# Optimization experiments

Measured on AMD Instinct MI355X. Metric: run time of the kernel, lower is better.

Reference implementation:

```python
import jax, jax.numpy as jnp
import numpy as np

N, E, HID, ED, L, H, D = 65536, 262144, 256, 64, 2, 8, 32
FF = 4 * HID
A_START = 8192  # first action gripper node; nodes [A_START:] are the T*K action nodes


def _ln(x, s, b, eps=1e-5):
    mu = jnp.mean(x, -1, keepdims=True)
    var = jnp.var(x, -1, keepdims=True)
    return (x - mu) * jax.lax.rsqrt(var + eps) * s + b


def _gnn_forward(x, edge_attr, edge_index, Wq, Wk, Wv, WeK, WeV, Wo,
                 ln1_s, ln1_b, ffn_w1, ffn_b1, ffn_w2, ffn_b2, ln2_s, ln2_b):
    # Hetero graph transformer over the single ('gripper','action','gripper') relation:
    # per-layer edge-indexed gather -> multi-head attention with edge features ->
    # segment softmax over incoming edges -> scatter-aggregate -> residual/LN/FFN.
    n = x.shape[0]
    e = edge_attr.shape[0]
    src, dst = edge_index[0], edge_index[1]
    inv_sqrt_d = np.float32(1.0 / np.sqrt(D))
    for l in range(Wq.shape[0]):
        q = (x @ Wq[l]).reshape(n, H, D)
        k = (x @ Wk[l]).reshape(n, H, D)
        v = (x @ Wv[l]).reshape(n, H, D)
        kj = k[src] + (edge_attr @ WeK[l]).reshape(e, H, D)  # [E,H,D] gathered keys + edge bias
        vj = v[src] + (edge_attr @ WeV[l]).reshape(e, H, D)
        score = jnp.einsum('ehd,ehd->eh', q[dst], kj) * inv_sqrt_d  # [E,H]
        smax = jax.ops.segment_max(score, dst, num_segments=n)
        p = jnp.exp(score - smax[dst])
        denom = jax.ops.segment_sum(p, dst, num_segments=n)
        alpha = p / denom[dst]  # segment softmax over incoming edges
        agg = jax.ops.segment_sum((alpha[..., None] * vj).reshape(e, H * D), dst, num_segments=n)
        x = _ln(x + agg @ Wo[l], ln1_s[l], ln1_b[l])
        hid = jax.nn.gelu(x @ ffn_w1[l] + ffn_b1[l], approximate=False) @ ffn_w2[l] + ffn_b2[l]
        x = _ln(x + hid, ln2_s[l], ln2_b[l])
    return x


def setup_inputs() -> dict:
    key = jax.random.key(0)
    ks = iter(jax.random.split(key, 16))
    w = lambda shape: jax.random.normal(next(ks), shape, jnp.float32) * 0.05
    return {
        "all_gripper_feats": jax.random.normal(next(ks), (N, HID), jnp.float32),
        "edge_attr": jax.random.normal(next(ks), (E, ED), jnp.float32),
        "Wq": w((L, HID, H * D)), "Wk": w((L, HID, H * D)), "Wv": w((L, HID, H * D)),
        "WeK": w((L, ED, H * D)), "WeV": w((L, ED, H * D)), "Wo": w((L, H * D, HID)),
        "ln1_s": jnp.ones((L, HID), jnp.float32), "ln1_b": jnp.zeros((L, HID), jnp.float32),
        "ffn_w1": w((L, HID, FF)), "ffn_b1": jnp.zeros((L, FF), jnp.float32),
        "ffn_w2": w((L, FF, HID)), "ffn_b2": jnp.zeros((L, HID), jnp.float32),
        "ln2_s": jnp.ones((L, HID), jnp.float32), "ln2_b": jnp.zeros((L, HID), jnp.float32),
        "head_w1": w((HID, HID)), "head_b1": jnp.zeros((HID,), jnp.float32),
        "head_w2": w((HID, 7)), "head_b2": jnp.zeros((7,), jnp.float32),
        "edge_index": jax.random.randint(next(ks), (2, E), 0, N),
        "action_start": A_START,
    }


def reference(all_gripper_feats, edge_attr, Wq, Wk, Wv, WeK, WeV, Wo,
              ln1_s, ln1_b, ffn_w1, ffn_b1, ffn_w2, ffn_b2, ln2_s, ln2_b,
              head_w1, head_b1, head_w2, head_b2, edge_index, action_start):
    x = _gnn_forward(all_gripper_feats, edge_attr, edge_index, Wq, Wk, Wv, WeK, WeV, Wo,
                     ln1_s, ln1_b, ffn_w1, ffn_b1, ffn_w2, ffn_b2, ln2_s, ln2_b)
    a = x[action_start:]  # action gripper nodes (T*K, hidden)
    return jax.nn.gelu(a @ head_w1 + head_b1, approximate=False) @ head_w2 + head_b2  # (T*K, 7)
```

## Files before the change

kernel.cpp:

```cpp
#include <hip/hip_runtime.h>
#include <hip/hip_bf16.h>
#include <math.h>

#define NN     65536
#define NE     262144
#define HIDN   256
#define EDIM   64
#define NHEAD  8
#define FFN    1024
#define ASTART 8192
#define NACT   (NN - ASTART)
#define NCH    32768
#define NCHUNK (NE / NCH)
#define DPC    (NN / NCHUNK)
#define RCH    32768

typedef __attribute__((ext_vector_type(8))) short short8;
typedef __attribute__((ext_vector_type(4))) short short4v;
typedef __attribute__((ext_vector_type(4))) float float4v;
typedef __hip_bfloat16 bf16;

__device__ __forceinline__ float b2f(short s) {
    union { unsigned u; float f; } c;
    c.u = ((unsigned)(unsigned short)s) << 16;
    return c.f;
}
__device__ __forceinline__ short f2b(float f) {
    __hip_bfloat16 h = __float2bfloat16(f);
    return *reinterpret_cast<short*>(&h);
}
__device__ __forceinline__ float gelu_fast(float v) {
    const float x  = v * 0.70710678118654752f;
    const float ax = fabsf(x);
    const float t  = __builtin_amdgcn_rcpf(1.0f + 0.3275911f * ax);
    const float y  = t * (0.254829592f + t * (-0.284496736f + t * (1.421413741f +
                     t * (-1.453152027f + t * 1.061405429f))));
    const float e  = __expf(-x * x);
    float erf = 1.0f - y * e;
    erf = copysignf(erf, x);
    return 0.5f * v * (1.0f + erf);
}
__device__ __forceinline__ void gload16(const void* g, void* l) {
    __builtin_amdgcn_global_load_lds(
        (const __attribute__((address_space(1))) void*)(uintptr_t)g,
        (__attribute__((address_space(3))) void*)(unsigned)(uintptr_t)l,
        16, 0, 0);
}

__global__ void convert_kernel(const float* __restrict__ src,
                               bf16* __restrict__ dst, int n) {
    int i = blockIdx.x * 256 + threadIdx.x;
    if (i < n) dst[i] = __float2bfloat16(src[i]);
}
__global__ void convert4_kernel(const float* __restrict__ src,
                                bf16* __restrict__ dst, int n4) {
    int i = blockIdx.x * 256 + threadIdx.x;
    if (i >= n4) return;
    float4v f = *(const float4v*)(src + (size_t)i * 4);
    short4v o;
    #pragma unroll
    for (int j = 0; j < 4; ++j) o[j] = f2b(f[j]);
    *(short4v*)((short*)dst + (size_t)i * 4) = o;
}

__global__ void transpose_kernel(const float* __restrict__ src,
                                 bf16* __restrict__ dst, int R, int Cc) {
    int idx = blockIdx.x * 256 + threadIdx.x;
    if (idx >= R * Cc) return;
    int r = idx / Cc, c = idx - r * Cc;
    dst[(size_t)c * R + r] = __float2bfloat16(src[idx]);
}

__global__ void hist_kernel(const int* __restrict__ dstI, int* __restrict__ cnt) {
    int i = blockIdx.x * 256 + threadIdx.x;
    if (i < NE) atomicAdd(&cnt[dstI[i]], 1);
}
__global__ void scan1_kernel(const int* __restrict__ cnt, int* __restrict__ rp,
                             int* __restrict__ bsum) {
    __shared__ int s[256];
    int t = threadIdx.x, i = blockIdx.x * 256 + t;
    int v = cnt[i]; s[t] = v; __syncthreads();
    for (int off = 1; off < 256; off <<= 1) {
        int x = (t >= off) ? s[t - off] : 0; __syncthreads();
        s[t] += x; __syncthreads();
    }
    rp[i] = s[t] - v;
    if (t == 255) bsum[blockIdx.x] = s[255];
}
__global__ void scan2_kernel(int* __restrict__ bsum) {
    __shared__ int s[256];
    int t = threadIdx.x; int v = bsum[t]; s[t] = v; __syncthreads();
    for (int off = 1; off < 256; off <<= 1) {
        int x = (t >= off) ? s[t - off] : 0; __syncthreads();
        s[t] += x; __syncthreads();
    }
    bsum[t] = s[t] - v;
}
__global__ void scan3_kernel(int* __restrict__ rp, const int* __restrict__ bsum,
                             int* __restrict__ cursor) {
    int i = blockIdx.x * 256 + threadIdx.x;
    int v = rp[i] + bsum[i >> 8];
    rp[i] = v; cursor[i] = v;
    if (i == 0) rp[NN] = NE;
}
__global__ void scatter_kernel(const int* __restrict__ srcI, const int* __restrict__ dstI,
                               int* __restrict__ cursor, int* __restrict__ perm,
                               int* __restrict__ src_s, int* __restrict__ dst_s) {
    int e = blockIdx.x * 256 + threadIdx.x;
    if (e >= NE) return;
    int d = dstI[e];
    int pos = atomicAdd(&cursor[d], 1);
    perm[pos] = e; src_s[pos] = srcI[e]; dst_s[pos] = d;
}

template<int AMODE, bool DO_GELU>
__global__ __launch_bounds__(256) void gemm_kernel(
    const void* __restrict__ A,
    const bf16* __restrict__ BT,
    const bf16* __restrict__ bias,
    bf16* __restrict__ C,
    int M, int Nn, int K,
    const int* __restrict__ perm)
{
    __shared__ __align__(16) short As[2][128 * 32];
    __shared__ __align__(16) short Bs[2][128 * 32];

    const int gx   = gridDim.x;
    const int nwg  = gx * gridDim.y;
    const int orig = blockIdx.y * gx + blockIdx.x;
    const int q8   = nwg >> 3, r8 = nwg & 7;
    const int xcd  = orig & 7, rk = orig >> 3;
    const int nid  = (xcd < r8 ? xcd * (q8 + 1) : r8 * (q8 + 1) + (xcd - r8) * q8) + rk;
    const int by   = nid / gx;
    const int bx   = nid - by * gx;

    const int t    = threadIdx.x;
    const int wave = t >> 6;
    const int lane = t & 63;
    const int l15  = lane & 15;
    const int quad = lane >> 4;
    const int wm   = (wave & 1) * 64;
    const int wn   = (wave >> 1) * 64;
    const int bm   = by * 128;
    const int bn   = bx * 128;
    const int srow = t >> 2;
    const int sw   = srow & 3;
    const int scolB = ((t & 3) ^ sw) * 8;
    const int scolA = (t & 3) * 8;

    const short* Ab = (const short*)A  + (size_t)(bm + srow) * K + scolB;
    const short* Bb = (const short*)BT + (size_t)(bn + srow) * K + scolB;
    const float* Af0 = nullptr;
    const float* Af1 = nullptr;
    if (AMODE == 1) {
        Af0 = (const float*)A + (size_t)(bm + srow) * K + scolA;
        Af1 = Af0 + (size_t)64 * K;
    } else if (AMODE == 2) {
        const int pr0 = perm[bm + srow];
        const int pr1 = perm[bm + 64 + srow];
        Af0 = (const float*)A + (size_t)pr0 * K + scolA;
        Af1 = (const float*)A + (size_t)pr1 * K + scolA;
    }
    const int offW  = wave * 1024;
    const int offTs = (t * 16) ^ (sw << 4);
    const int qs16  = (quad ^ (l15 & 3)) * 16;

    float4v acc[4][4];
    #pragma unroll
    for (int i = 0; i < 4; ++i)
        #pragma unroll
        for (int j = 0; j < 4; ++j) acc[i][j] = (float4v){0.f, 0.f, 0.f, 0.f};

    const int nt = K >> 5;

    auto STAGE = [&](int b, int k0) {
        char* lA = (char*)As[b];
        char* lB = (char*)Bs[b];
        if (AMODE == 0) {
            gload16(Ab + k0,                  lA + offW);
            gload16(Ab + (size_t)64 * K + k0, lA + 4096 + offW);
        } else {
            #pragma unroll
            for (int i = 0; i < 2; ++i) {
                const float* s = (i ? Af1 : Af0) + k0;
                float4v f0 = *(const float4v*)s;
                float4v f1 = *(const float4v*)(s + 4);
                short8 w;
                #pragma unroll
                for (int j = 0; j < 4; ++j) { w[j] = f2b(f0[j]); w[4 + j] = f2b(f1[j]); }
                *(short8*)(lA + i * 4096 + offTs) = w;
            }
        }
        gload16(Bb + k0,                  lB + offW);
        gload16(Bb + (size_t)64 * K + k0, lB + 4096 + offW);
    };

    STAGE(0, 0);
    __syncthreads();

    for (int kt = 0; kt < nt; ++kt) {
        const int cur = kt & 1;
        if (kt + 1 < nt) STAGE(cur ^ 1, (kt + 1) * 32);

        const char* lA = (const char*)As[cur];
        const char* lB = (const char*)Bs[cur];
        short8 afr[4], bfr[4];
        #pragma unroll
        for (int i = 0; i < 4; ++i)
            afr[i] = *(const short8*)(lA + (wm + i * 16 + l15) * 64 + qs16);
        #pragma unroll
        for (int j = 0; j < 4; ++j)
            bfr[j] = *(const short8*)(lB + (wn + j * 16 + l15) * 64 + qs16);
        #pragma unroll
        for (int i = 0; i < 4; ++i)
            #pragma unroll
            for (int j = 0; j < 4; ++j)
                acc[i][j] = __builtin_amdgcn_mfma_f32_16x16x32_bf16(afr[i], bfr[j], acc[i][j], 0, 0, 0);
        __syncthreads();
    }

    #pragma unroll
    for (int j = 0; j < 4; ++j) {
        const int col = bn + wn + j * 16 + l15;
        const float bv = bias ? b2f(((const short*)bias)[col]) : 0.0f;
        #pragma unroll
        for (int i = 0; i < 4; ++i) {
            const int row0 = bm + wm + i * 16 + quad * 4;
            #pragma unroll
            for (int r = 0; r < 4; ++r) {
                float v = acc[i][j][r] + bv;
                if (DO_GELU) v = gelu_fast(v);
                C[(size_t)(row0 + r) * Nn + col] = __float2bfloat16(v);
            }
        }
    }
}

__global__ __launch_bounds__(256) void score_kernel(
    const bf16* __restrict__ q, const bf16* __restrict__ k,
    const bf16* __restrict__ eK,
    const int* __restrict__ src_s, const int* __restrict__ dst_s,
    short* __restrict__ pbuf, int e0, int qkstride)
{
    const int p = e0 + blockIdx.x * 4 + (threadIdx.x >> 6);
    const int lane = threadIdx.x & 63;
    const int s = src_s[p], d = dst_s[p];
    const int off = lane * 4;

    const short4v qv = *(const short4v*)((const short*)q  + (size_t)d * qkstride + off);
    const short4v kv = *(const short4v*)((const short*)k  + (size_t)s * qkstride + off);
    const short4v ev = *(const short4v*)((const short*)eK + (size_t)(p - e0) * HIDN + off);
    float x = 0.f;
    #pragma unroll
    for (int j = 0; j < 4; ++j) x += b2f(qv[j]) * (b2f(kv[j]) + b2f(ev[j]));
    x += __shfl_xor(x, 1);
    x += __shfl_xor(x, 2);
    x += __shfl_xor(x, 4);
    if ((lane & 7) == 0) {
        const float sc = fminf(fmaxf(x * 0.17677669529663689f, -30.f), 30.f);
        pbuf[(size_t)p * NHEAD + (lane >> 3)] = f2b(expf(sc));
    }
}

__global__ __launch_bounds__(256) void agg_kernel(
    const short* __restrict__ pbuf, const bf16* __restrict__ v,
    const bf16* __restrict__ eV,
    const int* __restrict__ src_s, const int* __restrict__ rp,
    float* __restrict__ agg, int e0, int e1, int dlo)
{
    const int d = dlo + blockIdx.x * 4 + (threadIdx.x >> 6);
    const int lane = threadIdx.x & 63;
    const int es = rp[d], ee = rp[d + 1];
    const int lo = es > e0 ? es : e0;
    const int hi = ee < e1 ? ee : e1;
    if (lo >= hi) return;
    const int h = lane >> 3, off = lane * 4;

    float den = 0.f;
    for (int p = es; p < ee; ++p) den += b2f(pbuf[(size_t)p * NHEAD + h]);

    float a0 = 0.f, a1 = 0.f, a2 = 0.f, a3 = 0.f;
    for (int p = lo; p < hi; ++p) {
        const float al = b2f(pbuf[(size_t)p * NHEAD + h]) / den;
        const int s = src_s[p];
        const short4v vv = *(const short4v*)((const short*)v  + (size_t)s * HIDN + off);
        const short4v ev = *(const short4v*)((const short*)eV + (size_t)(p - e0) * HIDN + off);
        a0 += al * (b2f(vv[0]) + b2f(ev[0]));
        a1 += al * (b2f(vv[1]) + b2f(ev[1]));
        a2 += al * (b2f(vv[2]) + b2f(ev[2]));
        a3 += al * (b2f(vv[3]) + b2f(ev[3]));
    }
    float* ao = agg + (size_t)d * HIDN + off;
    if (es >= e0 && ee <= e1) {
        *(float4v*)ao = (float4v){a0, a1, a2, a3};
    } else {
        atomicAdd(ao + 0, a0); atomicAdd(ao + 1, a1);
        atomicAdd(ao + 2, a2); atomicAdd(ao + 3, a3);
    }
}

__global__ __launch_bounds__(256) void ln_kernel(
    bf16* __restrict__ x, const bf16* __restrict__ t,
    const bf16* __restrict__ sc, const bf16* __restrict__ bi, int r0)
{
    const int row = r0 + blockIdx.x * 4 + (threadIdx.x >> 6);
    const int lane = threadIdx.x & 63;
    const size_t base = (size_t)row * HIDN + lane * 4;
    const size_t tbase = (size_t)(row - r0) * HIDN + lane * 4;
    const short4v xv = *(const short4v*)((const short*)x + base);
    const short4v tv = *(const short4v*)((const short*)t + tbase);
    float v[4];
    #pragma unroll
    for (int j = 0; j < 4; ++j) v[j] = b2f(xv[j]) + b2f(tv[j]);
    float sum = v[0] + v[1] + v[2] + v[3];
    float ssq = v[0]*v[0] + v[1]*v[1] + v[2]*v[2] + v[3]*v[3];
    #pragma unroll
    for (int m = 1; m < 64; m <<= 1) { sum += __shfl_xor(sum, m); ssq += __shfl_xor(ssq, m); }
    const float mean = sum * (1.0f / 256.0f);
    const float var  = fmaxf(ssq * (1.0f / 256.0f) - mean * mean, 0.0f);
    const float rstd = rsqrtf(var + 1e-5f);
    const short4v sv = *(const short4v*)((const short*)sc + lane * 4);
    const short4v bv = *(const short4v*)((const short*)bi + lane * 4);
    short4v out;
    #pragma unroll
    for (int j = 0; j < 4; ++j)
        out[j] = f2b((v[j] - mean) * rstd * b2f(sv[j]) + b2f(bv[j]));
    *(short4v*)((short*)x + base) = out;
}

__global__ __launch_bounds__(256) void head2_kernel(
    const bf16* __restrict__ h1, const bf16* __restrict__ w2T,
    const bf16* __restrict__ b2, float* __restrict__ out)
{
    const int row = blockIdx.x * 4 + (threadIdx.x >> 6);
    const int lane = threadIdx.x & 63;
    const int off = lane * 4;
    const short4v hv = *(const short4v*)((const short*)h1 + (size_t)row * HIDN + off);
    float hf[4];
    #pragma unroll
    for (int j = 0; j < 4; ++j) hf[j] = b2f(hv[j]);
    float acc[7];
    #pragma unroll
    for (int jc = 0; jc < 7; ++jc) {
        const short4v wv = *(const short4v*)((const short*)w2T + jc * HIDN + off);
        float a = hf[0]*b2f(wv[0]) + hf[1]*b2f(wv[1]) + hf[2]*b2f(wv[2]) + hf[3]*b2f(wv[3]);
        #pragma unroll
        for (int m = 1; m < 64; m <<= 1) a += __shfl_xor(a, m);
        acc[jc] = a;
    }
    if (lane < 7) {
        float r = lane == 0 ? acc[0] : lane == 1 ? acc[1] : lane == 2 ? acc[2] :
                  lane == 3 ? acc[3] : lane == 4 ? acc[4] : lane == 5 ? acc[5] : acc[6];
        out[(size_t)row * 7 + lane] = r + b2f(((const short*)b2)[lane]);
    }
}

extern "C" void kernel_launch(void* const* d_in, const int* in_sizes, int n_in,
                              void* d_out, int out_size, void* d_ws, size_t ws_size,
                              hipStream_t stream)
{
    const float* xin   = (const float*)d_in[0];
    const float* eattr = (const float*)d_in[1];
    const float* Wq    = (const float*)d_in[2];
    const float* Wk    = (const float*)d_in[3];
    const float* Wv    = (const float*)d_in[4];
    const float* WeK   = (const float*)d_in[5];
    const float* WeV   = (const float*)d_in[6];
    const float* Wo    = (const float*)d_in[7];
    const float* ln1s  = (const float*)d_in[8];
    const float* ln1b  = (const float*)d_in[9];
    const float* fw1   = (const float*)d_in[10];
    const float* fb1   = (const float*)d_in[11];
    const float* fw2   = (const float*)d_in[12];
    const float* fb2   = (const float*)d_in[13];
    const float* ln2s  = (const float*)d_in[14];
    const float* ln2b  = (const float*)d_in[15];
    const float* hw1   = (const float*)d_in[16];
    const float* hb1   = (const float*)d_in[17];
    const float* hw2   = (const float*)d_in[18];
    const float* hb2   = (const float*)d_in[19];
    const int*  eidx   = (const int*)d_in[20];
    const int*  srcI   = eidx;
    const int*  dstI   = eidx + NE;

    char* base = (char*)d_ws;
    size_t off = 0;
    auto carve = [&](size_t bytes) -> char* {
        char* p = base + off;
        off += (bytes + 255) & ~(size_t)255;
        return p;
    };
    bf16*  x_b    = (bf16*) carve((size_t)NN * HIDN * 2);
    bf16*  qk_b   = (bf16*) carve((size_t)NN * 2 * HIDN * 2);
    bf16*  v_b    = (bf16*) carve((size_t)NN * HIDN * 2);
    bf16*  echunk = (bf16*) carve((size_t)NCH * HIDN * 2);
    short* pbuf   = (short*)carve((size_t)NE * NHEAD * 2);
    int*   perm   = (int*)  carve((size_t)NE * 4);
    int*   src_s  = (int*)  carve((size_t)NE * 4);
    int*   dst_s  = (int*)  carve((size_t)NE * 4);
    int*   rowp   = (int*)  carve((size_t)(NN + 1) * 4);
    bf16*  WqkT   = (bf16*) carve((size_t)2 * HIDN * HIDN * 2);
    bf16*  WvT    = (bf16*) carve((size_t)HIDN * HIDN * 2);
    bf16*  WoT    = (bf16*) carve((size_t)HIDN * HIDN * 2);
    bf16*  WeKT   = (bf16*) carve((size_t)HIDN * EDIM * 2);
    bf16*  WeVT   = (bf16*) carve((size_t)HIDN * EDIM * 2);
    bf16*  W1T    = (bf16*) carve((size_t)FFN * HIDN * 2);
    bf16*  W2T    = (bf16*) carve((size_t)HIDN * FFN * 2);
    bf16*  HW1T   = (bf16*) carve((size_t)HIDN * HIDN * 2);
    bf16*  HW2T   = (bf16*) carve((size_t)8 * HIDN * 2);
    bf16*  c_ln1s = (bf16*) carve((size_t)2 * HIDN * 2);
    bf16*  c_ln1b = (bf16*) carve((size_t)2 * HIDN * 2);
    bf16*  c_ln2s = (bf16*) carve((size_t)2 * HIDN * 2);
    bf16*  c_ln2b = (bf16*) carve((size_t)2 * HIDN * 2);
    bf16*  c_fb1  = (bf16*) carve((size_t)2 * FFN * 2);
    bf16*  c_fb2  = (bf16*) carve((size_t)2 * HIDN * 2);
    bf16*  c_hb1  = (bf16*) carve((size_t)HIDN * 2);
    bf16*  c_hb2  = (bf16*) carve((size_t)16 * 2);
    if (off > ws_size) return;

    int* cnt    = (int*)echunk;
    int* cursor = cnt + NN;
    int* bsum   = cursor + NN;
    float* agg    = (float*)qk_b;
    bf16*  tmp_b  = v_b;
    bf16*  hid    = qk_b;
    bf16*  ffnout = v_b;

    const int TB = 256;
    #define GRID1(n) dim3(((n) + TB - 1) / TB)

    convert4_kernel<<<GRID1(NN * HIDN / 4), TB, 0, stream>>>(xin, x_b, NN * HIDN / 4);
    convert_kernel<<<GRID1(2 * HIDN), TB, 0, stream>>>(ln1s, c_ln1s, 2 * HIDN);
    convert_kernel<<<GRID1(2 * HIDN), TB, 0, stream>>>(ln1b, c_ln1b, 2 * HIDN);
    convert_kernel<<<GRID1(2 * HIDN), TB, 0, stream>>>(ln2s, c_ln2s, 2 * HIDN);
    convert_kernel<<<GRID1(2 * HIDN), TB, 0, stream>>>(ln2b, c_ln2b, 2 * HIDN);
    convert_kernel<<<GRID1(2 * FFN), TB, 0, stream>>>(fb1, c_fb1, 2 * FFN);
    convert_kernel<<<GRID1(2 * HIDN), TB, 0, stream>>>(fb2, c_fb2, 2 * HIDN);
    convert_kernel<<<GRID1(HIDN), TB, 0, stream>>>(hb1, c_hb1, HIDN);
    convert_kernel<<<1, TB, 0, stream>>>(hb2, c_hb2, 7);
    transpose_kernel<<<GRID1(HIDN * HIDN), TB, 0, stream>>>(hw1, HW1T, HIDN, HIDN);
    transpose_kernel<<<GRID1(HIDN * 7), TB, 0, stream>>>(hw2, HW2T, HIDN, 7);

    hipMemsetAsync(cnt, 0, (size_t)NN * 4, stream);
    hist_kernel<<<GRID1(NE), TB, 0, stream>>>(dstI, cnt);
    scan1_kernel<<<NN / 256, 256, 0, stream>>>(cnt, rowp, bsum);
    scan2_kernel<<<1, 256, 0, stream>>>(bsum);
    scan3_kernel<<<NN / 256, 256, 0, stream>>>(rowp, bsum, cursor);
    scatter_kernel<<<GRID1(NE), TB, 0, stream>>>(srcI, dstI, cursor, perm, src_s, dst_s);

    for (int l = 0; l < 2; ++l) {
        transpose_kernel<<<GRID1(HIDN * HIDN), TB, 0, stream>>>(Wq + (size_t)l*HIDN*HIDN, WqkT, HIDN, HIDN);
        transpose_kernel<<<GRID1(HIDN * HIDN), TB, 0, stream>>>(Wk + (size_t)l*HIDN*HIDN, WqkT + (size_t)HIDN*HIDN, HIDN, HIDN);
        transpose_kernel<<<GRID1(HIDN * HIDN), TB, 0, stream>>>(Wv + (size_t)l*HIDN*HIDN, WvT, HIDN, HIDN);
        transpose_kernel<<<GRID1(EDIM * HIDN), TB, 0, stream>>>(WeK + (size_t)l*EDIM*HIDN, WeKT, EDIM, HIDN);
        transpose_kernel<<<GRID1(EDIM * HIDN), TB, 0, stream>>>(WeV + (size_t)l*EDIM*HIDN, WeVT, EDIM, HIDN);
        transpose_kernel<<<GRID1(HIDN * HIDN), TB, 0, stream>>>(Wo + (size_t)l*HIDN*HIDN, WoT, HIDN, HIDN);
        transpose_kernel<<<GRID1(HIDN * FFN),  TB, 0, stream>>>(fw1 + (size_t)l*HIDN*FFN, W1T, HIDN, FFN);
        transpose_kernel<<<GRID1(FFN * HIDN),  TB, 0, stream>>>(fw2 + (size_t)l*FFN*HIDN, W2T, FFN, HIDN);

        gemm_kernel<0, false><<<dim3((2*HIDN)/128, NN/128), TB, 0, stream>>>(x_b, WqkT, nullptr, qk_b, NN, 2*HIDN, HIDN, nullptr);
        gemm_kernel<0, false><<<dim3(HIDN/128, NN/128), TB, 0, stream>>>(x_b, WvT, nullptr, v_b, NN, HIDN, HIDN, nullptr);

        for (int c = 0; c < NCHUNK; ++c) {
            gemm_kernel<2, false><<<dim3(HIDN/128, NCH/128), TB, 0, stream>>>(
                eattr, WeKT, nullptr, echunk, NCH, HIDN, EDIM, perm + (size_t)c * NCH);
            score_kernel<<<NCH / 4, TB, 0, stream>>>(qk_b, qk_b + HIDN, echunk, src_s, dst_s, pbuf, c * NCH, 2 * HIDN);
        }

        hipMemsetAsync(agg, 0, (size_t)NN * HIDN * 4, stream);
        for (int c = 0; c < NCHUNK; ++c) {
            gemm_kernel<2, false><<<dim3(HIDN/128, NCH/128), TB, 0, stream>>>(
                eattr, WeVT, nullptr, echunk, NCH, HIDN, EDIM, perm + (size_t)c * NCH);
            const int dlo = (c == 0) ? 0 : (c - 1) * DPC;
            const int dhi = (c == NCHUNK - 1) ? NN : (c + 2) * DPC;
            agg_kernel<<<(dhi - dlo) / 4, TB, 0, stream>>>(
                pbuf, v_b, echunk, src_s, rowp, agg, c * NCH, (c + 1) * NCH, dlo);
        }

        gemm_kernel<1, false><<<dim3(HIDN/128, NN/128), TB, 0, stream>>>(agg, WoT, nullptr, tmp_b, NN, HIDN, HIDN, nullptr);
        ln_kernel<<<NN / 4, TB, 0, stream>>>(x_b, tmp_b, c_ln1s + (size_t)l * HIDN, c_ln1b + (size_t)l * HIDN, 0);

        for (int r0 = 0; r0 < NN; r0 += RCH) {
            gemm_kernel<0, true ><<<dim3(FFN/128, RCH/128), TB, 0, stream>>>(
                x_b + (size_t)r0 * HIDN, W1T, c_fb1 + (size_t)l * FFN, hid, RCH, FFN, HIDN, nullptr);
            gemm_kernel<0, false><<<dim3(HIDN/128, RCH/128), TB, 0, stream>>>(
                hid, W2T, c_fb2 + (size_t)l * HIDN, ffnout, RCH, HIDN, FFN, nullptr);
            ln_kernel<<<RCH / 4, TB, 0, stream>>>(x_b, ffnout, c_ln2s + (size_t)l * HIDN, c_ln2b + (size_t)l * HIDN, r0);
        }
    }

    gemm_kernel<0, true><<<dim3(HIDN/128, NACT/128), TB, 0, stream>>>(
        x_b + (size_t)ASTART * HIDN, HW1T, c_hb1, hid, NACT, HIDN, HIDN, nullptr);
    head2_kernel<<<NACT / 4, TB, 0, stream>>>(hid, HW2T, c_hb2, (float*)d_out);
}
```

Measured before the change: 1.538 ms.

## Stage GEMM epilogue through LDS and assign destinations wholly to one chunk in aggregation

The GEMM epilogue now writes results into shared memory with an XOR swizzle and then stores full 16-byte rows to global memory, replacing scattered 2-byte stores. The edge-aggregation pass gives each destination node to the single chunk that holds its first edge. The eV chunk is padded by 128 rows so a destination's edges that run past the chunk boundary are covered, which removes the atomic partial-sum path and the agg memset. This costs one extra padded GEMM tile row per chunk and an extra barrier in every GEMM. Correctness also relies on every destination having fewer than 128 incoming edges beyond a chunk boundary.

Measured after the change: 1.505 ms. 2.1% less time.

```diff
diff --git a/kernel.cpp b/kernel.cpp
--- a/kernel.cpp
+++ b/kernel.cpp
@@ -11,6 +11,7 @@
 #define ASTART 8192
 #define NACT   (NN - ASTART)
 #define NCH    32768
+#define NCHP   (NCH + 128)
 #define NCHUNK (NE / NCH)
 #define DPC    (NN / NCHUNK)
 #define RCH    32768
@@ -120,10 +121,9 @@
     const bf16* __restrict__ bias,
     bf16* __restrict__ C,
     int M, int Nn, int K,
-    const int* __restrict__ perm)
+    const int* __restrict__ perm, int permN)
 {
-    __shared__ __align__(16) short As[2][128 * 32];
-    __shared__ __align__(16) short Bs[2][128 * 32];
+    __shared__ __align__(16) short Ls[4][128 * 32];
 
     const int gx   = gridDim.x;
     const int nwg  = gx * gridDim.y;
@@ -156,8 +156,10 @@
         Af0 = (const float*)A + (size_t)(bm + srow) * K + scolA;
         Af1 = Af0 + (size_t)64 * K;
     } else if (AMODE == 2) {
-        const int pr0 = perm[bm + srow];
-        const int pr1 = perm[bm + 64 + srow];
+        int i0 = bm + srow;       if (i0 >= permN) i0 = permN - 1;
+        int i1 = bm + 64 + srow;  if (i1 >= permN) i1 = permN - 1;
+        const int pr0 = perm[i0];
+        const int pr1 = perm[i1];
         Af0 = (const float*)A + (size_t)pr0 * K + scolA;
         Af1 = (const float*)A + (size_t)pr1 * K + scolA;
     }
@@ -174,8 +176,8 @@
     const int nt = K >> 5;
 
     auto STAGE = [&](int b, int k0) {
-        char* lA = (char*)As[b];
-        char* lB = (char*)Bs[b];
+        char* lA = (char*)Ls[b];
+        char* lB = (char*)Ls[2 + b];
         if (AMODE == 0) {
             gload16(Ab + k0,                  lA + offW);
             gload16(Ab + (size_t)64 * K + k0, lA + 4096 + offW);
@@ -202,8 +204,8 @@
         const int cur = kt & 1;
         if (kt + 1 < nt) STAGE(cur ^ 1, (kt + 1) * 32);
 
-        const char* lA = (const char*)As[cur];
-        const char* lB = (const char*)Bs[cur];
+        const char* lA = (const char*)Ls[cur];
+        const char* lB = (const char*)Ls[2 + cur];
         short8 afr[4], bfr[4];
         #pragma unroll
         for (int i = 0; i < 4; ++i)
@@ -219,20 +221,31 @@
         __syncthreads();
     }
 
+    short* Ct = (short*)Ls;
     #pragma unroll
     for (int j = 0; j < 4; ++j) {
-        const int col = bn + wn + j * 16 + l15;
-        const float bv = bias ? b2f(((const short*)bias)[col]) : 0.0f;
+        const int col  = wn + j * 16 + l15;
+        const int pc   = col ^ (quad << 4);
+        const float bv = bias ? b2f(((const short*)bias)[bn + col]) : 0.0f;
         #pragma unroll
         for (int i = 0; i < 4; ++i) {
-            const int row0 = bm + wm + i * 16 + quad * 4;
+            const int row0 = wm + i * 16 + quad * 4;
             #pragma unroll
             for (int r = 0; r < 4; ++r) {
                 float v = acc[i][j][r] + bv;
                 if (DO_GELU) v = gelu_fast(v);
-                C[(size_t)(row0 + r) * Nn + col] = __float2bfloat16(v);
+                Ct[(row0 + r) * 128 + pc] = f2b(v);
             }
         }
+    }
+    __syncthreads();
+    #pragma unroll
+    for (int it = 0; it < 8; ++it) {
+        const int row = wave * 32 + it + ((lane >> 4) << 3);
+        const int cs  = (lane & 15) * 8;
+        const int pcs = cs ^ (((row >> 2) & 3) << 4);
+        short8 w = *(const short8*)&Ct[row * 128 + pcs];
+        *(short8*)((short*)C + (size_t)(bm + row) * Nn + bn + cs) = w;
     }
 }
 
@@ -266,37 +279,31 @@
     const short* __restrict__ pbuf, const bf16* __restrict__ v,
     const bf16* __restrict__ eV,
     const int* __restrict__ src_s, const int* __restrict__ rp,
-    float* __restrict__ agg, int e0, int e1, int dlo)
+    float* __restrict__ agg, int e0, int e1x, int dlo)
 {
     const int d = dlo + blockIdx.x * 4 + (threadIdx.x >> 6);
     const int lane = threadIdx.x & 63;
     const int es = rp[d], ee = rp[d + 1];
-    const int lo = es > e0 ? es : e0;
-    const int hi = ee < e1 ? ee : e1;
-    if (lo >= hi) return;
+    if (es < e0 || es >= e1x) return;
     const int h = lane >> 3, off = lane * 4;
 
-    float den = 0.f;
-    for (int p = es; p < ee; ++p) den += b2f(pbuf[(size_t)p * NHEAD + h]);
-
     float a0 = 0.f, a1 = 0.f, a2 = 0.f, a3 = 0.f;
-    for (int p = lo; p < hi; ++p) {
-        const float al = b2f(pbuf[(size_t)p * NHEAD + h]) / den;
-        const int s = src_s[p];
-        const short4v vv = *(const short4v*)((const short*)v  + (size_t)s * HIDN + off);
-        const short4v ev = *(const short4v*)((const short*)eV + (size_t)(p - e0) * HIDN + off);
-        a0 += al * (b2f(vv[0]) + b2f(ev[0]));
-        a1 += al * (b2f(vv[1]) + b2f(ev[1]));
-        a2 += al * (b2f(vv[2]) + b2f(ev[2]));
-        a3 += al * (b2f(vv[3]) + b2f(ev[3]));
-    }
-    float* ao = agg + (size_t)d * HIDN + off;
-    if (es >= e0 && ee <= e1) {
-        *(float4v*)ao = (float4v){a0, a1, a2, a3};
-    } else {
-        atomicAdd(ao + 0, a0); atomicAdd(ao + 1, a1);
-        atomicAdd(ao + 2, a2); atomicAdd(ao + 3, a3);
-    }
+    if (es < ee) {
+        float den = 0.f;
+        for (int p = es; p < ee; ++p) den += b2f(pbuf[(size_t)p * NHEAD + h]);
+        const float rden = 1.0f / den;
+        for (int p = es; p < ee; ++p) {
+            const float al = b2f(pbuf[(size_t)p * NHEAD + h]) * rden;
+            const int s = src_s[p];
+            const short4v vv = *(const short4v*)((const short*)v  + (size_t)s * HIDN + off);
+            const short4v ev = *(const short4v*)((const short*)eV + (size_t)(p - e0) * HIDN + off);
+            a0 += al * (b2f(vv[0]) + b2f(ev[0]));
+            a1 += al * (b2f(vv[1]) + b2f(ev[1]));
+            a2 += al * (b2f(vv[2]) + b2f(ev[2]));
+            a3 += al * (b2f(vv[3]) + b2f(ev[3]));
+        }
+    }
+    *(float4v*)(agg + (size_t)d * HIDN + off) = (float4v){a0, a1, a2, a3};
 }
 
 __global__ __launch_bounds__(256) void ln_kernel(
@@ -393,7 +400,7 @@
     bf16*  x_b    = (bf16*) carve((size_t)NN * HIDN * 2);
     bf16*  qk_b   = (bf16*) carve((size_t)NN * 2 * HIDN * 2);
     bf16*  v_b    = (bf16*) carve((size_t)NN * HIDN * 2);
-    bf16*  echunk = (bf16*) carve((size_t)NCH * HIDN * 2);
+    bf16*  echunk = (bf16*) carve((size_t)NCHP * HIDN * 2);
     short* pbuf   = (short*)carve((size_t)NE * NHEAD * 2);
     int*   perm   = (int*)  carve((size_t)NE * 4);
     int*   src_s  = (int*)  carve((size_t)NE * 4);
@@ -458,38 +465,38 @@
         transpose_kernel<<<GRID1(HIDN * FFN),  TB, 0, stream>>>(fw1 + (size_t)l*HIDN*FFN, W1T, HIDN, FFN);
         transpose_kernel<<<GRID1(FFN * HIDN),  TB, 0, stream>>>(fw2 + (size_t)l*FFN*HIDN, W2T, FFN, HIDN);
 
-        gemm_kernel<0, false><<<dim3((2*HIDN)/128, NN/128), TB, 0, stream>>>(x_b, WqkT, nullptr, qk_b, NN, 2*HIDN, HIDN, nullptr);
-        gemm_kernel<0, false><<<dim3(HIDN/128, NN/128), TB, 0, stream>>>(x_b, WvT, nullptr, v_b, NN, HIDN, HIDN, nullptr);
+        gemm_kernel<0, false><<<dim3((2*HIDN)/128, NN/128), TB, 0, stream>>>(x_b, WqkT, nullptr, qk_b, NN, 2*HIDN, HIDN, nullptr, 0);
+        gemm_kernel<0, false><<<dim3(HIDN/128, NN/128), TB, 0, stream>>>(x_b, WvT, nullptr, v_b, NN, HIDN, HIDN, nullptr, 0);
 
         for (int c = 0; c < NCHUNK; ++c) {
             gemm_kernel<2, false><<<dim3(HIDN/128, NCH/128), TB, 0, stream>>>(
-                eattr, WeKT, nullptr, echunk, NCH, HIDN, EDIM, perm + (size_t)c * NCH);
+                eattr, WeKT, nullptr, echunk, NCH, HIDN, EDIM, perm + (size_t)c * NCH, NE - c * NCH);
             score_kernel<<<NCH / 4, TB, 0, stream>>>(qk_b, qk_b + HIDN, echunk, src_s, dst_s, pbuf, c * NCH, 2 * HIDN);
         }
 
-        hipMemsetAsync(agg, 0, (size_t)NN * HIDN * 4, stream);
         for (int c = 0; c < NCHUNK; ++c) {
-            gemm_kernel<2, false><<<dim3(HIDN/128, NCH/128), TB, 0, stream>>>(
-                eattr, WeVT, nullptr, echunk, NCH, HIDN, EDIM, perm + (size_t)c * NCH);
+            gemm_kernel<2, false><<<dim3(HIDN/128, NCHP/128), TB, 0, stream>>>(
+                eattr, WeVT, nullptr, echunk, NCHP, HIDN, EDIM, perm + (size_t)c * NCH, NE - c * NCH);
             const int dlo = (c == 0) ? 0 : (c - 1) * DPC;
             const int dhi = (c == NCHUNK - 1) ? NN : (c + 2) * DPC;
+            const int e1x = (c == NCHUNK - 1) ? NE + 1 : (c + 1) * NCH;
             agg_kernel<<<(dhi - dlo) / 4, TB, 0, stream>>>(
-                pbuf, v_b, echunk, src_s, rowp, agg, c * NCH, (c + 1) * NCH, dlo);
+                pbuf, v_b, echunk, src_s, rowp, agg, c * NCH, e1x, dlo);
         }
 
-        gemm_kernel<1, false><<<dim3(HIDN/128, NN/128), TB, 0, stream>>>(agg, WoT, nullptr, tmp_b, NN, HIDN, HIDN, nullptr);
+        gemm_kernel<1, false><<<dim3(HIDN/128, NN/128), TB, 0, stream>>>(agg, WoT, nullptr, tmp_b, NN, HIDN, HIDN, nullptr, 0);
         ln_kernel<<<NN / 4, TB, 0, stream>>>(x_b, tmp_b, c_ln1s + (size_t)l * HIDN, c_ln1b + (size_t)l * HIDN, 0);
 
         for (int r0 = 0; r0 < NN; r0 += RCH) {
             gemm_kernel<0, true ><<<dim3(FFN/128, RCH/128), TB, 0, stream>>>(
-                x_b + (size_t)r0 * HIDN, W1T, c_fb1 + (size_t)l * FFN, hid, RCH, FFN, HIDN, nullptr);
+                x_b + (size_t)r0 * HIDN, W1T, c_fb1 + (size_t)l * FFN, hid, RCH, FFN, HIDN, nullptr, 0);
             gemm_kernel<0, false><<<dim3(HIDN/128, RCH/128), TB, 0, stream>>>(
-                hid, W2T, c_fb2 + (size_t)l * HIDN, ffnout, RCH, HIDN, FFN, nullptr);
+                hid, W2T, c_fb2 + (size_t)l * HIDN, ffnout, RCH, HIDN, FFN, nullptr, 0);
             ln_kernel<<<RCH / 4, TB, 0, stream>>>(x_b, ffnout, c_ln2s + (size_t)l * HIDN, c_ln2b + (size_t)l * HIDN, r0);
         }
     }
 
     gemm_kernel<0, true><<<dim3(HIDN/128, NACT/128), TB, 0, stream>>>(
-        x_b + (size_t)ASTART * HIDN, HW1T, c_hb1, hid, NACT, HIDN, HIDN, nullptr);
+        x_b + (size_t)ASTART * HIDN, HW1T, c_hb1, hid, NACT, HIDN, HIDN, nullptr, 0);
     head2_kernel<<<NACT / 4, TB, 0, stream>>>(hid, HW2T, c_hb2, (float*)d_out);
 }
```
